# Optimization experiments

Hardware: AMD Instinct MI355X
Metric: run time of the kernel (lower is better)

## Reference

```python
import jax, jax.numpy as jnp
import numpy as np

NEG_INF = -1e9


def setup_inputs() -> dict:
    key = jax.random.key(0)
    k1, k2, k3, k4 = jax.random.split(key, 4)
    N, F_in, F_out = 8192, 512, 256
    features = jax.random.normal(k1, (N, F_in), dtype=jnp.float32)
    adj = jax.random.randint(k2, (N, N), 0, 2).astype(jnp.float32)
    W = jax.random.normal(k3, (F_in, F_out), dtype=jnp.float32) * 0.05
    a = jax.random.normal(k4, (2 * F_out,), dtype=jnp.float32) * 0.05
    return {"features": features, "adj": adj, "W": W, "a": a}


def reference(features, adj, W, a):
    # h = W @ features  -> [N, F_out]
    h = features @ W
    F_out = h.shape[1]
    a_src, a_dst = a[:F_out], a[F_out:]
    # a^T [h_i ; h_j] decomposes into per-node dot products (same math as
    # the concat+linear in the original, without the [N,N,2F] intermediate).
    e = jax.nn.leaky_relu((h @ a_src)[:, None] + (h @ a_dst)[None, :],
                          negative_slope=0.01)  # [N, N]
    masked_e = e + NEG_INF * (1.0 - adj)
    attention = jax.nn.softmax(masked_e, axis=1)  # row-wise over neighbors j
    output = attention @ h  # [N, F_out]
    return output, attention
```

## Files before the change

### kernel.cpp

```cpp
#include <hip/hip_runtime.h>
#include <hip/hip_bf16.h>

#define N 8192
#define FIN 512
#define FOUT 256

typedef __attribute__((ext_vector_type(8))) short bf16x8;
typedef __attribute__((ext_vector_type(4))) float f32x4;

__device__ __forceinline__ unsigned short f2bf(float x) {
  unsigned int u = __float_as_uint(x);
  return (unsigned short)((u + 0x7FFFu + ((u >> 16) & 1u)) >> 16);
}

__global__ __launch_bounds__(256) void gat_k1_gemm_h(
    const float* __restrict__ A, const float* __restrict__ W,
    float* __restrict__ h, unsigned short* __restrict__ hT) {
  __shared__ __align__(16) float As[16][68];
  __shared__ __align__(16) float Bs[16][64];
  const int tid = threadIdx.x;
  const int tx = tid & 15, ty = tid >> 4;
  const int nb = blockIdx.x * 64, mb = blockIdx.y * 64;
  float acc[4][4] = {};
  for (int k0 = 0; k0 < FIN; k0 += 16) {
#pragma unroll
    for (int i = 0; i < 4; ++i) {
      int e = tid + 256 * i;
      int m = e >> 4, k = e & 15;
      As[k][m] = A[(size_t)(mb + m) * FIN + k0 + k];
      int n2 = e & 63, k2 = e >> 6;
      Bs[k2][n2] = W[(size_t)(k0 + k2) * FOUT + nb + n2];
    }
    __syncthreads();
#pragma unroll
    for (int k = 0; k < 16; ++k) {
      float4 av = *reinterpret_cast<const float4*>(&As[k][ty * 4]);
      float4 bv = *reinterpret_cast<const float4*>(&Bs[k][tx * 4]);
      float aa[4] = {av.x, av.y, av.z, av.w};
      float bb[4] = {bv.x, bv.y, bv.z, bv.w};
#pragma unroll
      for (int i = 0; i < 4; ++i)
#pragma unroll
        for (int j = 0; j < 4; ++j) acc[i][j] = fmaf(aa[i], bb[j], acc[i][j]);
    }
    __syncthreads();
  }
#pragma unroll
  for (int i = 0; i < 4; ++i) {
    int m = mb + ty * 4 + i;
#pragma unroll
    for (int j = 0; j < 4; ++j) {
      int n = nb + tx * 4 + j;
      h[(size_t)m * FOUT + n] = acc[i][j];
      hT[(size_t)n * N + m] = f2bf(acc[i][j]);
    }
  }
}

__global__ __launch_bounds__(256) void gat_k2_hshd(
    const float* __restrict__ h, const float* __restrict__ a,
    float* __restrict__ hs, float* __restrict__ hd) {
  const int wid = threadIdx.x >> 6;
  const int lane = threadIdx.x & 63;
  const int row = blockIdx.x * 4 + wid;
  float ps = 0.f, pd = 0.f;
#pragma unroll
  for (int i = 0; i < 4; ++i) {
    int c = lane + 64 * i;
    float v = h[(size_t)row * FOUT + c];
    ps += v * a[c];
    pd += v * a[FOUT + c];
  }
#pragma unroll
  for (int off = 32; off >= 1; off >>= 1) {
    ps += __shfl_down(ps, off);
    pd += __shfl_down(pd, off);
  }
  if (lane == 0) {
    hs[row] = ps;
    hd[row] = pd;
  }
}

__global__ __launch_bounds__(256) void gat_k3_attn(
    const float* __restrict__ adj, const float* __restrict__ hs,
    const float* __restrict__ hd, float* __restrict__ att) {
  __shared__ __align__(16) float hd_s[N];
  __shared__ float red[4];
  const int tid = threadIdx.x;
  const int lane = tid & 63, wid = tid >> 6;
#pragma unroll
  for (int i = 0; i < 8; ++i) {
    int j = tid * 4 + 1024 * i;
    *reinterpret_cast<float4*>(&hd_s[j]) =
        *reinterpret_cast<const float4*>(&hd[j]);
  }
  __syncthreads();
  const int row0 = blockIdx.x * 8;
  for (int r = 0; r < 8; ++r) {
    const int row = row0 + r;
    const float hsv = hs[row];
    const float* arow = adj + (size_t)row * N;
    float4 l[8];
    float m = -__builtin_inff();
#pragma unroll
    for (int i = 0; i < 8; ++i) {
      int j = tid * 4 + 1024 * i;
      float4 a4 = *reinterpret_cast<const float4*>(&arow[j]);
      float4 h4 = *reinterpret_cast<const float4*>(&hd_s[j]);
      float4 lv;
      float x;
      x = hsv + h4.x; x = x > 0.f ? x : 0.01f * x;
      lv.x = (a4.x != 0.f) ? x : -__builtin_inff();
      x = hsv + h4.y; x = x > 0.f ? x : 0.01f * x;
      lv.y = (a4.y != 0.f) ? x : -__builtin_inff();
      x = hsv + h4.z; x = x > 0.f ? x : 0.01f * x;
      lv.z = (a4.z != 0.f) ? x : -__builtin_inff();
      x = hsv + h4.w; x = x > 0.f ? x : 0.01f * x;
      lv.w = (a4.w != 0.f) ? x : -__builtin_inff();
      l[i] = lv;
      m = fmaxf(m, fmaxf(fmaxf(lv.x, lv.y), fmaxf(lv.z, lv.w)));
    }
#pragma unroll
    for (int off = 32; off >= 1; off >>= 1) m = fmaxf(m, __shfl_down(m, off));
    if (lane == 0) red[wid] = m;
    __syncthreads();
    m = fmaxf(fmaxf(red[0], red[1]), fmaxf(red[2], red[3]));
    __syncthreads();
    float s = 0.f;
#pragma unroll
    for (int i = 0; i < 8; ++i) {
      float4 lv = l[i];
      lv.x = __expf(lv.x - m);
      lv.y = __expf(lv.y - m);
      lv.z = __expf(lv.z - m);
      lv.w = __expf(lv.w - m);
      l[i] = lv;
      s += lv.x + lv.y + lv.z + lv.w;
    }
#pragma unroll
    for (int off = 32; off >= 1; off >>= 1) s += __shfl_down(s, off);
    if (lane == 0) red[wid] = s;
    __syncthreads();
    s = red[0] + red[1] + red[2] + red[3];
    __syncthreads();
    const float inv = 1.f / s;
    float* orow = att + (size_t)row * N;
#pragma unroll
    for (int i = 0; i < 8; ++i) {
      float4 lv = l[i];
      lv.x *= inv; lv.y *= inv; lv.z *= inv; lv.w *= inv;
      *reinterpret_cast<float4*>(&orow[tid * 4 + 1024 * i]) = lv;
    }
  }
}

__global__ __launch_bounds__(512) void gat_k4_out(
    const float* __restrict__ att, const unsigned short* __restrict__ hT,
    float* __restrict__ C) {
  __shared__ __align__(16) unsigned short As[2][32 * 64];
  __shared__ __align__(16) unsigned short Bs[2][256 * 64];
  const int tid = threadIdx.x;
  const int lane = tid & 63;
  const int wn = tid >> 6;
  const int mb = blockIdx.x * 32;
  const int g = lane >> 4, rsel = lane & 15;
  const int ar = tid >> 4, ap = tid & 15;
  const float* asrc = att + (size_t)(mb + ar) * N + ap * 4;
  const int abyte = ar * 128 + ((ap * 8) ^ ((ar & 7) << 4));
  const unsigned short* bsrc[4];
  int bbyte[4];
#pragma unroll
  for (int i = 0; i < 4; ++i) {
    int s = tid + 512 * i;
    int n = s >> 3, kg = s & 7;
    int kgs = kg ^ (n & 7);
    bsrc[i] = hT + (size_t)n * N + kgs * 8;
    bbyte[i] = s * 16;
  }

  f32x4 acc[2][2] = {};
  float4 aA;
  uint4 bB0, bB1, bB2, bB3;

  aA = *reinterpret_cast<const float4*>(asrc);
  bB0 = *reinterpret_cast<const uint4*>(bsrc[0]);
  bB1 = *reinterpret_cast<const uint4*>(bsrc[1]);
  bB2 = *reinterpret_cast<const uint4*>(bsrc[2]);
  bB3 = *reinterpret_cast<const uint4*>(bsrc[3]);
  {
    uint2 pk;
    pk.x = (unsigned)f2bf(aA.x) | ((unsigned)f2bf(aA.y) << 16);
    pk.y = (unsigned)f2bf(aA.z) | ((unsigned)f2bf(aA.w) << 16);
    *reinterpret_cast<uint2*>(reinterpret_cast<char*>(As[0]) + abyte) = pk;
    *reinterpret_cast<uint4*>(reinterpret_cast<char*>(Bs[0]) + bbyte[0]) = bB0;
    *reinterpret_cast<uint4*>(reinterpret_cast<char*>(Bs[0]) + bbyte[1]) = bB1;
    *reinterpret_cast<uint4*>(reinterpret_cast<char*>(Bs[0]) + bbyte[2]) = bB2;
    *reinterpret_cast<uint4*>(reinterpret_cast<char*>(Bs[0]) + bbyte[3]) = bB3;
  }

  int cur = 0;
  for (int t = 0; t < 128; ++t) {
    const int knext = (t + 1) * 64;
    if (t < 127) {
      aA = *reinterpret_cast<const float4*>(asrc + knext);
      bB0 = *reinterpret_cast<const uint4*>(bsrc[0] + knext);
      bB1 = *reinterpret_cast<const uint4*>(bsrc[1] + knext);
      bB2 = *reinterpret_cast<const uint4*>(bsrc[2] + knext);
      bB3 = *reinterpret_cast<const uint4*>(bsrc[3] + knext);
    }
    __syncthreads();
    const char* Ac = reinterpret_cast<const char*>(As[cur]);
    const char* Bc = reinterpret_cast<const char*>(Bs[cur]);
#pragma unroll
    for (int ks = 0; ks < 2; ++ks) {
      bf16x8 af[2], bg[2];
#pragma unroll
      for (int f = 0; f < 2; ++f) {
        int r = f * 16 + rsel;
        af[f] = *reinterpret_cast<const bf16x8*>(
            Ac + r * 128 + ((ks * 64 + g * 16) ^ ((r & 7) << 4)));
        int n = wn * 32 + f * 16 + rsel;
        bg[f] = *reinterpret_cast<const bf16x8*>(
            Bc + n * 128 + ((ks * 64 + g * 16) ^ ((n & 7) << 4)));
      }
#pragma unroll
      for (int i = 0; i < 2; ++i)
#pragma unroll
        for (int j = 0; j < 2; ++j)
          acc[i][j] = __builtin_amdgcn_mfma_f32_16x16x32_bf16(af[i], bg[j],
                                                              acc[i][j], 0, 0, 0);
    }
    if (t < 127) {
      char* An = reinterpret_cast<char*>(As[cur ^ 1]);
      char* Bn = reinterpret_cast<char*>(Bs[cur ^ 1]);
      uint2 pk;
      pk.x = (unsigned)f2bf(aA.x) | ((unsigned)f2bf(aA.y) << 16);
      pk.y = (unsigned)f2bf(aA.z) | ((unsigned)f2bf(aA.w) << 16);
      *reinterpret_cast<uint2*>(An + abyte) = pk;
      *reinterpret_cast<uint4*>(Bn + bbyte[0]) = bB0;
      *reinterpret_cast<uint4*>(Bn + bbyte[1]) = bB1;
      *reinterpret_cast<uint4*>(Bn + bbyte[2]) = bB2;
      *reinterpret_cast<uint4*>(Bn + bbyte[3]) = bB3;
      cur ^= 1;
    }
  }
#pragma unroll
  for (int i = 0; i < 2; ++i)
#pragma unroll
    for (int j = 0; j < 2; ++j)
#pragma unroll
      for (int r = 0; r < 4; ++r) {
        int row = mb + i * 16 + g * 4 + r;
        int col = wn * 32 + j * 16 + rsel;
        C[(size_t)row * FOUT + col] = acc[i][j][r];
      }
}

extern "C" void kernel_launch(void* const* d_in, const int* in_sizes, int n_in,
                              void* d_out, int out_size, void* d_ws, size_t ws_size,
                              hipStream_t stream) {
  const float* features = (const float*)d_in[0];
  const float* adj = (const float*)d_in[1];
  const float* W = (const float*)d_in[2];
  const float* a = (const float*)d_in[3];

  float* out = (float*)d_out;
  float* att = out + (size_t)N * FOUT;

  char* ws = (char*)d_ws;
  float* h = (float*)ws;
  unsigned short* hT = (unsigned short*)(ws + (size_t)N * FOUT * 4);
  float* hs = (float*)(ws + (size_t)N * FOUT * 4 + (size_t)N * FOUT * 2);
  float* hd = hs + N;

  hipLaunchKernelGGL(gat_k1_gemm_h, dim3(FOUT / 64, N / 64), dim3(256), 0,
                     stream, features, W, h, hT);
  hipLaunchKernelGGL(gat_k2_hshd, dim3(N / 4), dim3(256), 0, stream, h, a, hs,
                     hd);
  hipLaunchKernelGGL(gat_k3_attn, dim3(N / 8), dim3(256), 0, stream, adj, hs,
                     hd, att);
  hipLaunchKernelGGL(gat_k4_out, dim3(N / 32), dim3(512), 0, stream, att, hT,
                     out);
}
```

Baseline: 272.8 us.

## Retile output GEMM to 128-row blocks with split-K and atomic accumulation

The attention@h kernel moves from 32-row blocks with 8 waves to 128x256 tiles with 16 waves. K is split into four 2048-wide chunks, and the mapping interleaves row blocks with K quarters. Partial results are combined with atomicAdd into an output that the hs/hd kernel now zeroes. The goal is to cut the repeated reloads of hT across row blocks, which happened 256 times before, while keeping 256 blocks for occupancy. The cost is atomic traffic, 1024-thread blocks with larger LDS use, and non-deterministic summation order.

Measured after the change: 232.4 us. 14.8% less time.

```diff
diff --git a/kernel.cpp b/kernel.cpp
--- a/kernel.cpp
+++ b/kernel.cpp
@@ -59,7 +59,11 @@
 
 __global__ __launch_bounds__(256) void gat_k2_hshd(
     const float* __restrict__ h, const float* __restrict__ a,
-    float* __restrict__ hs, float* __restrict__ hd) {
+    float* __restrict__ hs, float* __restrict__ hd, float* __restrict__ out) {
+  const int gid = blockIdx.x * 256 + threadIdx.x;
+  *reinterpret_cast<float4*>(out + (size_t)gid * 4) =
+      make_float4(0.f, 0.f, 0.f, 0.f);
+
   const int wid = threadIdx.x >> 6;
   const int lane = threadIdx.x & 63;
   const int row = blockIdx.x * 4 + wid;
@@ -155,105 +159,121 @@
   }
 }
 
-__global__ __launch_bounds__(512) void gat_k4_out(
+__global__ __launch_bounds__(1024) void gat_k4_out(
     const float* __restrict__ att, const unsigned short* __restrict__ hT,
     float* __restrict__ C) {
-  __shared__ __align__(16) unsigned short As[2][32 * 64];
+  __shared__ __align__(16) unsigned short As[2][128 * 64];
   __shared__ __align__(16) unsigned short Bs[2][256 * 64];
   const int tid = threadIdx.x;
   const int lane = tid & 63;
-  const int wn = tid >> 6;
-  const int mb = blockIdx.x * 32;
+  const int wid = tid >> 6;
+  const int wm = wid >> 2, wn = wid & 3;
   const int g = lane >> 4, rsel = lane & 15;
-  const int ar = tid >> 4, ap = tid & 15;
-  const float* asrc = att + (size_t)(mb + ar) * N + ap * 4;
-  const int abyte = ar * 128 + ((ap * 8) ^ ((ar & 7) << 4));
-  const unsigned short* bsrc[4];
-  int bbyte[4];
-#pragma unroll
-  for (int i = 0; i < 4; ++i) {
-    int s = tid + 512 * i;
+  const int id = blockIdx.x;
+  const int grp = id & 7, pos = id >> 3;
+  const int kq = grp & 3;
+  const int rb = (grp >> 2) + 2 * pos;
+  const int row0 = rb * 128;
+  const int kbase = kq * 2048;
+
+  const float* asrc[2];
+  int abyte[2];
+#pragma unroll
+  for (int i = 0; i < 2; ++i) {
+    int e = tid + 1024 * i;
+    int r = e >> 4, p = e & 15;
+    asrc[i] = att + (size_t)(row0 + r) * N + kbase + p * 4;
+    abyte[i] = r * 128 + ((p * 8) ^ ((r & 7) << 4));
+  }
+  const unsigned short* bsrc[2];
+  int bbyte[2];
+#pragma unroll
+  for (int i = 0; i < 2; ++i) {
+    int s = tid + 1024 * i;
     int n = s >> 3, kg = s & 7;
     int kgs = kg ^ (n & 7);
-    bsrc[i] = hT + (size_t)n * N + kgs * 8;
+    bsrc[i] = hT + (size_t)n * N + kbase + kgs * 8;
     bbyte[i] = s * 16;
   }
 
-  f32x4 acc[2][2] = {};
-  float4 aA;
-  uint4 bB0, bB1, bB2, bB3;
-
-  aA = *reinterpret_cast<const float4*>(asrc);
+  f32x4 acc[2][4] = {};
+  float4 aA0, aA1;
+  uint4 bB0, bB1;
+
+  aA0 = *reinterpret_cast<const float4*>(asrc[0]);
+  aA1 = *reinterpret_cast<const float4*>(asrc[1]);
   bB0 = *reinterpret_cast<const uint4*>(bsrc[0]);
   bB1 = *reinterpret_cast<const uint4*>(bsrc[1]);
-  bB2 = *reinterpret_cast<const uint4*>(bsrc[2]);
-  bB3 = *reinterpret_cast<const uint4*>(bsrc[3]);
   {
     uint2 pk;
-    pk.x = (unsigned)f2bf(aA.x) | ((unsigned)f2bf(aA.y) << 16);
-    pk.y = (unsigned)f2bf(aA.z) | ((unsigned)f2bf(aA.w) << 16);
-    *reinterpret_cast<uint2*>(reinterpret_cast<char*>(As[0]) + abyte) = pk;
+    pk.x = (unsigned)f2bf(aA0.x) | ((unsigned)f2bf(aA0.y) << 16);
+    pk.y = (unsigned)f2bf(aA0.z) | ((unsigned)f2bf(aA0.w) << 16);
+    *reinterpret_cast<uint2*>(reinterpret_cast<char*>(As[0]) + abyte[0]) = pk;
+    pk.x = (unsigned)f2bf(aA1.x) | ((unsigned)f2bf(aA1.y) << 16);
+    pk.y = (unsigned)f2bf(aA1.z) | ((unsigned)f2bf(aA1.w) << 16);
+    *reinterpret_cast<uint2*>(reinterpret_cast<char*>(As[0]) + abyte[1]) = pk;
     *reinterpret_cast<uint4*>(reinterpret_cast<char*>(Bs[0]) + bbyte[0]) = bB0;
     *reinterpret_cast<uint4*>(reinterpret_cast<char*>(Bs[0]) + bbyte[1]) = bB1;
-    *reinterpret_cast<uint4*>(reinterpret_cast<char*>(Bs[0]) + bbyte[2]) = bB2;
-    *reinterpret_cast<uint4*>(reinterpret_cast<char*>(Bs[0]) + bbyte[3]) = bB3;
   }
 
   int cur = 0;
-  for (int t = 0; t < 128; ++t) {
+  for (int t = 0; t < 32; ++t) {
     const int knext = (t + 1) * 64;
-    if (t < 127) {
-      aA = *reinterpret_cast<const float4*>(asrc + knext);
+    if (t < 31) {
+      aA0 = *reinterpret_cast<const float4*>(asrc[0] + knext);
+      aA1 = *reinterpret_cast<const float4*>(asrc[1] + knext);
       bB0 = *reinterpret_cast<const uint4*>(bsrc[0] + knext);
       bB1 = *reinterpret_cast<const uint4*>(bsrc[1] + knext);
-      bB2 = *reinterpret_cast<const uint4*>(bsrc[2] + knext);
-      bB3 = *reinterpret_cast<const uint4*>(bsrc[3] + knext);
     }
     __syncthreads();
     const char* Ac = reinterpret_cast<const char*>(As[cur]);
     const char* Bc = reinterpret_cast<const char*>(Bs[cur]);
 #pragma unroll
     for (int ks = 0; ks < 2; ++ks) {
-      bf16x8 af[2], bg[2];
+      bf16x8 af[2], bg[4];
 #pragma unroll
       for (int f = 0; f < 2; ++f) {
-        int r = f * 16 + rsel;
+        int r = wm * 32 + f * 16 + rsel;
         af[f] = *reinterpret_cast<const bf16x8*>(
             Ac + r * 128 + ((ks * 64 + g * 16) ^ ((r & 7) << 4)));
-        int n = wn * 32 + f * 16 + rsel;
+      }
+#pragma unroll
+      for (int f = 0; f < 4; ++f) {
+        int n = wn * 64 + f * 16 + rsel;
         bg[f] = *reinterpret_cast<const bf16x8*>(
             Bc + n * 128 + ((ks * 64 + g * 16) ^ ((n & 7) << 4)));
       }
 #pragma unroll
       for (int i = 0; i < 2; ++i)
 #pragma unroll
-        for (int j = 0; j < 2; ++j)
+        for (int j = 0; j < 4; ++j)
           acc[i][j] = __builtin_amdgcn_mfma_f32_16x16x32_bf16(af[i], bg[j],
                                                               acc[i][j], 0, 0, 0);
     }
-    if (t < 127) {
+    if (t < 31) {
       char* An = reinterpret_cast<char*>(As[cur ^ 1]);
       char* Bn = reinterpret_cast<char*>(Bs[cur ^ 1]);
       uint2 pk;
-      pk.x = (unsigned)f2bf(aA.x) | ((unsigned)f2bf(aA.y) << 16);
-      pk.y = (unsigned)f2bf(aA.z) | ((unsigned)f2bf(aA.w) << 16);
-      *reinterpret_cast<uint2*>(An + abyte) = pk;
+      pk.x = (unsigned)f2bf(aA0.x) | ((unsigned)f2bf(aA0.y) << 16);
+      pk.y = (unsigned)f2bf(aA0.z) | ((unsigned)f2bf(aA0.w) << 16);
+      *reinterpret_cast<uint2*>(An + abyte[0]) = pk;
+      pk.x = (unsigned)f2bf(aA1.x) | ((unsigned)f2bf(aA1.y) << 16);
+      pk.y = (unsigned)f2bf(aA1.z) | ((unsigned)f2bf(aA1.w) << 16);
+      *reinterpret_cast<uint2*>(An + abyte[1]) = pk;
       *reinterpret_cast<uint4*>(Bn + bbyte[0]) = bB0;
       *reinterpret_cast<uint4*>(Bn + bbyte[1]) = bB1;
-      *reinterpret_cast<uint4*>(Bn + bbyte[2]) = bB2;
-      *reinterpret_cast<uint4*>(Bn + bbyte[3]) = bB3;
       cur ^= 1;
     }
   }
 #pragma unroll
   for (int i = 0; i < 2; ++i)
 #pragma unroll
-    for (int j = 0; j < 2; ++j)
+    for (int j = 0; j < 4; ++j)
 #pragma unroll
       for (int r = 0; r < 4; ++r) {
-        int row = mb + i * 16 + g * 4 + r;
-        int col = wn * 32 + j * 16 + rsel;
-        C[(size_t)row * FOUT + col] = acc[i][j][r];
+        int row = row0 + wm * 32 + i * 16 + g * 4 + r;
+        int col = wn * 64 + j * 16 + rsel;
+        atomicAdd(&C[(size_t)row * FOUT + col], acc[i][j][r]);
       }
 }
 
@@ -277,9 +297,9 @@
   hipLaunchKernelGGL(gat_k1_gemm_h, dim3(FOUT / 64, N / 64), dim3(256), 0,
                      stream, features, W, h, hT);
   hipLaunchKernelGGL(gat_k2_hshd, dim3(N / 4), dim3(256), 0, stream, h, a, hs,
-                     hd);
+                     hd, out);
   hipLaunchKernelGGL(gat_k3_attn, dim3(N / 8), dim3(256), 0, stream, adj, hs,
                      hd, att);
-  hipLaunchKernelGGL(gat_k4_out, dim3(N / 32), dim3(512), 0, stream, att, hT,
+  hipLaunchKernelGGL(gat_k4_out, dim3(256), dim3(1024), 0, stream, att, hT,
                      out);
 }
```
